# Kernel optimization log

Hardware: AMD Instinct MI355X
Metric: run time of the kernel (lower is better)

## Reference

```python
import jax, jax.numpy as jnp
import numpy as np

LTH_THOLD = 0.0

def _mlp(x, w1, b1, w2, b2, w3, b3):
    # x: [b,h,s,d]; w*: [h,in,out]; per-head 3-layer MLP with SiLU
    h1 = jax.nn.silu(jnp.einsum('bhsd,hde->bhse', x, w1) + b1[None, :, None, :])
    h2 = jax.nn.silu(jnp.einsum('bhsd,hde->bhse', h1, w2) + b2[None, :, None, :])
    return jnp.einsum('bhsd,hde->bhse', h2, w3) + b3[None, :, None, :]

def setup_inputs() -> dict:
    key = jax.random.key(0)
    ks = jax.random.split(key, 16)
    b, h, s, d, idim, fdim = 2, 32, 2048, 128, 128, 32
    sc1 = 1.0 / np.sqrt(d); sc2 = 1.0 / np.sqrt(idim)
    def lin(k, fan_in, shape, sc):
        return jax.random.uniform(k, shape, jnp.float32, -sc, sc)
    inp = {
        'K': jax.random.normal(ks[0], (b, h, s, d), jnp.float32),
        'Q': jax.random.normal(ks[1], (b, h, s, d), jnp.float32),
        'wk1': lin(ks[2], d, (h, d, idim), sc1), 'bk1': lin(ks[3], d, (h, idim), sc1),
        'wk2': lin(ks[4], idim, (h, idim, idim), sc2), 'bk2': lin(ks[5], idim, (h, idim), sc2),
        'wk3': lin(ks[6], idim, (h, idim, fdim), sc2), 'bk3': lin(ks[7], idim, (h, fdim), sc2),
        'wq1': lin(ks[8], d, (h, d, idim), sc1), 'bq1': lin(ks[9], d, (h, idim), sc1),
        'wq2': lin(ks[10], idim, (h, idim, idim), sc2), 'bq2': lin(ks[11], idim, (h, idim), sc2),
        'wq3': lin(ks[12], idim, (h, idim, fdim), sc2), 'bq3': lin(ks[13], idim, (h, fdim), sc2),
    }
    return inp

def reference(K, Q, wk1, bk1, wk2, bk2, wk3, bk3, wq1, bq1, wq2, bq2, wq3, bq3):
    Klift = jnp.tanh(_mlp(K, wk1, bk1, wk2, bk2, wk3, bk3))  # [b,h,sk,32]
    Qlift = jnp.tanh(_mlp(Q, wq1, bq1, wq2, bq2, wq3, bq3))  # [b,h,sq,32]
    scores = jnp.einsum('bhtd,bhsd->bhts', Qlift, Klift)      # [b,h,sq,sk]
    sq, sk = Qlift.shape[2], Klift.shape[2]
    causal = jnp.tril(jnp.ones((sq, sk), bool), k=sk - sq)
    mask_value = jnp.finfo(scores.dtype).min
    scores = jnp.where(causal[None, None], scores, mask_value)
    scores = jax.nn.sigmoid(scores - LTH_THOLD)
    return (scores, Klift)
```

## Files before the change

### kernel.cpp

```cpp
#include <hip/hip_runtime.h>

typedef __attribute__((ext_vector_type(8))) short bf16x8;
typedef __attribute__((ext_vector_type(4))) float f32x4;

#define MFMA(a,b,c) __builtin_amdgcn_mfma_f32_16x16x32_bf16(a,b,c,0,0,0)

static __device__ __forceinline__ unsigned short f2bf(float f){
  unsigned u = __float_as_uint(f);
  u += 0x7FFF + ((u>>16)&1);
  return (unsigned short)(u>>16);
}
static __device__ __forceinline__ float bf2f(unsigned short b){
  return __uint_as_float(((unsigned)b)<<16);
}

__global__ __launch_bounds__(256) void wswz(
    const float* __restrict__ wk1, const float* __restrict__ wk2, const float* __restrict__ wk3,
    const float* __restrict__ wq1, const float* __restrict__ wq2, const float* __restrict__ wq3,
    unsigned short* __restrict__ wb)
{
  int y = blockIdx.y;
  int net = y / 3, layer = y % 3;
  const float* src = net ? (layer==0?wq1: layer==1?wq2:wq3)
                         : (layer==0?wk1: layer==1?wk2:wk3);
  int N  = (layer==2) ? 32 : 128;
  int NT = N / 16;
  int total = 32 * NT * 4 * 64;
  int e = blockIdx.x * 256 + threadIdx.x;
  if (e >= total) return;
  int lane = e & 63;
  int ks   = (e >> 6) & 3;
  int nt   = (e >> 8) % NT;
  int h    = (e >> 8) / NT;
  int k0 = ks*32 + 8*(lane>>4);
  int n0 = nt*16 + (lane&15);
  const float* s = src + (size_t)h*128*N + (size_t)k0*N + n0;
  unsigned short hi[8], lo[8];
  #pragma unroll
  for (int j=0;j<8;++j){
    float v = s[(size_t)j*N];
    unsigned short hh = f2bf(v);
    hi[j] = hh;
    lo[j] = f2bf(v - bf2f(hh));
  }
  size_t nb   = (size_t)net * 2359296;
  size_t loff = (layer==0) ? 0 : (layer==1) ? 1048576 : 2097152;
  size_t losz = (layer==2) ? 131072 : 524288;
  size_t eidx = ((((size_t)h*NT + nt)*4 + ks)*64 + lane)*8;
  unsigned short* dH = wb + nb + loff + eidx;
  unsigned short* dL = dH + losz;
  *(bf16x8*)dH = *(const bf16x8*)hi;
  *(bf16x8*)dL = *(const bf16x8*)lo;
}

__global__ __launch_bounds__(256,3) void lift(
    const float* __restrict__ Kin, const float* __restrict__ Qin,
    const float* __restrict__ bk1, const float* __restrict__ bk2, const float* __restrict__ bk3,
    const float* __restrict__ bq1, const float* __restrict__ bq2, const float* __restrict__ bq3,
    const unsigned short* __restrict__ wb,
    unsigned short* __restrict__ qlift, unsigned short* __restrict__ klift,
    float* __restrict__ kout)
{
  __shared__ unsigned short XH[64][136];
  __shared__ unsigned short XL[64][136];
  int bid = blockIdx.x;
  int h   = (bid & 7)*4 + ((bid>>3)&3);
  int st  = (bid>>5) & 31;
  int bb  = (bid>>10) & 1;
  int net = bid>>11;
  size_t rowbase = (size_t)(bb*32 + h)*2048 + (size_t)st*64;
  const float* X = (net ? Qin : Kin) + rowbase*128;
  const unsigned short* wn = wb + (size_t)net*2359296;
  const float* b1 = (net ? bq1 : bk1) + h*128;
  const float* b2 = (net ? bq2 : bk2) + h*128;
  const float* b3 = (net ? bq3 : bk3) + h*32;
  unsigned short* lifto = net ? qlift : klift;

  int tid = threadIdx.x, w = tid >> 6, l = tid & 63;
  int lr = l & 15, lg = l >> 4;
  int acol0 = 8*lg;

  #pragma unroll
  for (int i=0;i<8;++i){
    int row = i*8 + (tid>>5);
    int col = (tid&31)*4;
    float4 v = *(const float4*)&X[(size_t)row*128 + col];
    unsigned u0=__float_as_uint(v.x), u1=__float_as_uint(v.y),
             u2=__float_as_uint(v.z), u3=__float_as_uint(v.w);
    float l0 = v.x - __uint_as_float(u0 & 0xFFFF0000u);
    float l1 = v.y - __uint_as_float(u1 & 0xFFFF0000u);
    float l2 = v.z - __uint_as_float(u2 & 0xFFFF0000u);
    float l3 = v.w - __uint_as_float(u3 & 0xFFFF0000u);
    *(uint2*)&XH[row][col] = make_uint2((u0>>16) | (u1 & 0xFFFF0000u),
                                        (u2>>16) | (u3 & 0xFFFF0000u));
    *(uint2*)&XL[row][col] = make_uint2((__float_as_uint(l0)>>16) | (__float_as_uint(l1) & 0xFFFF0000u),
                                        (__float_as_uint(l2)>>16) | (__float_as_uint(l3) & 0xFFFF0000u));
  }
  __syncthreads();

  for (int L=0; L<2; ++L){
    const unsigned short* wH = wn + (size_t)L*1048576;
    const unsigned short* wL = wH + 524288;
    const float* bias = L ? b2 : b1;
    f32x4 acc[2][4];
    #pragma unroll
    for (int ntl=0;ntl<2;++ntl)
      #pragma unroll
      for (int rt=0;rt<4;++rt)
        acc[ntl][rt] = (f32x4){0.f,0.f,0.f,0.f};

    #pragma unroll
    for (int ks=0;ks<4;++ks){
      bf16x8 bh[2], bl[2];
      #pragma unroll
      for (int ntl=0;ntl<2;++ntl){
        size_t eidx = ((((size_t)h*8 + (w*2+ntl))*4 + ks)*64 + l)*8;
        bh[ntl] = *(const bf16x8*)(wH + eidx);
        bl[ntl] = *(const bf16x8*)(wL + eidx);
      }
      #pragma unroll
      for (int rt=0;rt<4;++rt){
        bf16x8 ah = *(const bf16x8*)&XH[rt*16+lr][ks*32 + acol0];
        bf16x8 al = *(const bf16x8*)&XL[rt*16+lr][ks*32 + acol0];
        #pragma unroll
        for (int ntl=0;ntl<2;++ntl){
          f32x4 a = acc[ntl][rt];
          a = MFMA(bh[ntl], ah, a);
          a = MFMA(bh[ntl], al, a);
          a = MFMA(bl[ntl], ah, a);
          acc[ntl][rt] = a;
        }
      }
    }
    __syncthreads();
    #pragma unroll
    for (int ntl=0;ntl<2;++ntl){
      int n0 = (w*2+ntl)*16 + 4*lg;
      float4 bv = *(const float4*)&bias[n0];
      float bvv[4] = {bv.x, bv.y, bv.z, bv.w};
      #pragma unroll
      for (int rt=0;rt<4;++rt){
        int row = rt*16 + lr;
        unsigned hh[4], ll[4];
        #pragma unroll
        for (int i=0;i<4;++i){
          float v = acc[ntl][rt][i] + bvv[i];
          float sg = v * __builtin_amdgcn_rcpf(1.f + __expf(-v));
          unsigned u = __float_as_uint(sg);
          hh[i] = u >> 16;
          float lo = sg - __uint_as_float(u & 0xFFFF0000u);
          ll[i] = __float_as_uint(lo) >> 16;
        }
        *(uint2*)&XH[row][n0] = make_uint2(hh[0] | (hh[1]<<16), hh[2] | (hh[3]<<16));
        *(uint2*)&XL[row][n0] = make_uint2(ll[0] | (ll[1]<<16), ll[2] | (ll[3]<<16));
      }
    }
    __syncthreads();
  }

  {
    const unsigned short* wH = wn + 2097152;
    const unsigned short* wL = wH + 131072;
    int nt = w >> 1;
    int rb = (w & 1) * 2;
    f32x4 acc3[2];
    acc3[0] = (f32x4){0.f,0.f,0.f,0.f};
    acc3[1] = (f32x4){0.f,0.f,0.f,0.f};
    #pragma unroll
    for (int ks=0;ks<4;++ks){
      size_t eidx = ((((size_t)h*2 + nt)*4 + ks)*64 + l)*8;
      bf16x8 bh = *(const bf16x8*)(wH + eidx);
      bf16x8 bl = *(const bf16x8*)(wL + eidx);
      #pragma unroll
      for (int j=0;j<2;++j){
        bf16x8 ah = *(const bf16x8*)&XH[(rb+j)*16+lr][ks*32 + acol0];
        bf16x8 al = *(const bf16x8*)&XL[(rb+j)*16+lr][ks*32 + acol0];
        f32x4 a = acc3[j];
        a = MFMA(bh, ah, a);
        a = MFMA(bh, al, a);
        a = MFMA(bl, ah, a);
        acc3[j] = a;
      }
    }
    int n0 = nt*16 + 4*lg;
    float4 bv = *(const float4*)&b3[n0];
    float bvv[4] = {bv.x, bv.y, bv.z, bv.w};
    #pragma unroll
    for (int j=0;j<2;++j){
      int row = (rb+j)*16 + lr;
      float t4[4];
      unsigned short hb[4];
      #pragma unroll
      for (int i=0;i<4;++i){
        float v = acc3[j][i] + bvv[i];
        float e2 = __expf(2.f*v);
        float t  = 1.f - 2.f*__builtin_amdgcn_rcpf(e2 + 1.f);
        t4[i] = t;
        hb[i] = f2bf(t);
      }
      size_t gro = (rowbase + (size_t)row)*32 + n0;
      *(uint2*)&lifto[gro] = make_uint2((unsigned)hb[0] | ((unsigned)hb[1]<<16),
                                        (unsigned)hb[2] | ((unsigned)hb[3]<<16));
      if (net == 0)
        *(float4*)&kout[gro] = make_float4(t4[0], t4[1], t4[2], t4[3]);
    }
  }
}

__global__ __launch_bounds__(256) void scores_k(
    const unsigned short* __restrict__ qlift,
    const unsigned short* __restrict__ klift,
    float* __restrict__ out)
{
  int orig = blockIdx.x;
  int bid  = (orig & 7) * 2048 + (orig >> 3);
  int tc = bid & 15, tr = (bid >> 4) & 15, bh = bid >> 8;
  size_t sbase = (size_t)bh * 2048 * 2048;
  int r0 = tr * 128, c0 = tc * 128;
  int tid = threadIdx.x;

  if (tc > tr){
    float4 z = {0.f,0.f,0.f,0.f};
    #pragma unroll
    for (int it=0; it<16; ++it){
      int idx = it*256 + tid;
      int row = idx >> 5, c4 = idx & 31;
      *(float4*)&out[sbase + (size_t)(r0+row)*2048 + c0 + c4*4] = z;
    }
    return;
  }

  __shared__ float sbuf[4][16][128];
  int w = tid >> 6, l = tid & 63;
  int lr = l & 15, lg = l >> 4;
  int acol0 = 8*lg;
  float* sw = &sbuf[w][0][0];

  const unsigned short* qb = qlift + ((size_t)bh*2048 + r0 + w*32)*32;
  bf16x8 q0 = *(const bf16x8*)(qb + (size_t)lr*32 + acol0);
  bf16x8 q1 = *(const bf16x8*)(qb + (size_t)(16+lr)*32 + acol0);
  bool diag = (tc == tr);

  const unsigned short* kb = klift + ((size_t)bh*2048 + c0)*32;
  bf16x8 kf[8];
  #pragma unroll
  for (int st8=0; st8<8; ++st8)
    kf[st8] = *(const bf16x8*)(kb + (size_t)(st8*16+lr)*32 + acol0);

  #pragma unroll
  for (int pass=0; pass<2; ++pass){
    bf16x8 qf = pass ? q1 : q0;
    int tbase = r0 + w*32 + pass*16;
    int t = tbase + lr;

    #pragma unroll
    for (int st8=0; st8<8; ++st8){
      f32x4 z4 = {0.f,0.f,0.f,0.f};
      f32x4 d = MFMA(kf[st8], qf, z4);
      int scol = c0 + st8*16 + 4*lg;
      f32x4 p;
      #pragma unroll
      for (int i=0;i<4;++i){
        float pv = __builtin_amdgcn_rcpf(1.f + __expf(-d[i]));
        if (diag && (scol + i > t)) pv = 0.f;
        p[i] = pv;
      }
      int fi = (lr*128 + st8*16 + lg*4) ^ ((lr&7)<<2);
      *(f32x4*)&sw[fi] = p;
    }
    #pragma unroll
    for (int it=0; it<8; ++it){
      int r  = it*2 + (l>>5);
      int fi = (r*128 + (l&31)*4) ^ ((r&7)<<2);
      f32x4 v = *(const f32x4*)&sw[fi];
      *(f32x4*)&out[sbase + (size_t)(tbase + r)*2048 + c0 + (l&31)*4] = v;
    }
  }
}

extern "C" void kernel_launch(void* const* d_in, const int* in_sizes, int n_in,
                              void* d_out, int out_size, void* d_ws, size_t ws_size,
                              hipStream_t stream) {
  const float* K   = (const float*)d_in[0];
  const float* Q   = (const float*)d_in[1];
  const float* wk1 = (const float*)d_in[2];  const float* bk1 = (const float*)d_in[3];
  const float* wk2 = (const float*)d_in[4];  const float* bk2 = (const float*)d_in[5];
  const float* wk3 = (const float*)d_in[6];  const float* bk3 = (const float*)d_in[7];
  const float* wq1 = (const float*)d_in[8];  const float* bq1 = (const float*)d_in[9];
  const float* wq2 = (const float*)d_in[10]; const float* bq2 = (const float*)d_in[11];
  const float* wq3 = (const float*)d_in[12]; const float* bq3 = (const float*)d_in[13];
  float* out = (float*)d_out;

  unsigned short* ws    = (unsigned short*)d_ws;
  unsigned short* qlift = ws;
  unsigned short* klift = ws + 4194304;
  unsigned short* wbase = ws + 8388608;

  hipLaunchKernelGGL(wswz, dim3(256,6), dim3(256), 0, stream,
                     wk1, wk2, wk3, wq1, wq2, wq3, wbase);
  hipLaunchKernelGGL(lift, dim3(4096), dim3(256), 0, stream,
                     K, Q, bk1, bk2, bk3, bq1, bq2, bq3,
                     wbase, qlift, klift, out + 268435456ull);
  hipLaunchKernelGGL(scores_k, dim3(16384), dim3(256), 0, stream,
                     qlift, klift, out);
}
```

Baseline: 279.6 us.

## Remap scores kernel to row-strip blocks with waves striding column tiles

The scores kernel now gives each block a 16-row strip covering all 2048 columns. Each of the four waves walks every fourth 128-column tile, computing the causal tiles and writing zeros for the masked ones. Previously each block owned a 128x128 tile. The change balances causal versus zero-fill work within every block, so no blocks exist that only store zeros, and it halves the grid. The cost is that each wave reloads K fragments per tile from global memory, and Q reuse across the block drops.

```diff
diff --git a/kernel.cpp b/kernel.cpp
--- a/kernel.cpp
+++ b/kernel.cpp
@@ -213,67 +213,58 @@
     float* __restrict__ out)
 {
   int orig = blockIdx.x;
-  int bid  = (orig & 7) * 2048 + (orig >> 3);
-  int tc = bid & 15, tr = (bid >> 4) & 15, bh = bid >> 8;
-  size_t sbase = (size_t)bh * 2048 * 2048;
-  int r0 = tr * 128, c0 = tc * 128;
-  int tid = threadIdx.x;
-
-  if (tc > tr){
-    float4 z = {0.f,0.f,0.f,0.f};
-    #pragma unroll
-    for (int it=0; it<16; ++it){
-      int idx = it*256 + tid;
-      int row = idx >> 5, c4 = idx & 31;
-      *(float4*)&out[sbase + (size_t)(r0+row)*2048 + c0 + c4*4] = z;
-    }
-    return;
-  }
-
-  __shared__ float sbuf[4][16][128];
-  int w = tid >> 6, l = tid & 63;
+  int bid  = (orig & 7) * 1024 + (orig >> 3);
+  int sl = bid & 127;
+  int bh = bid >> 7;
+  int T0 = sl * 16;
+  int diagW = sl >> 3;
+  int tid = threadIdx.x, w = tid >> 6, l = tid & 63;
   int lr = l & 15, lg = l >> 4;
   int acol0 = 8*lg;
+
+  __shared__ float sbuf[4][16][128];
   float* sw = &sbuf[w][0][0];
 
-  const unsigned short* qb = qlift + ((size_t)bh*2048 + r0 + w*32)*32;
-  bf16x8 q0 = *(const bf16x8*)(qb + (size_t)lr*32 + acol0);
-  bf16x8 q1 = *(const bf16x8*)(qb + (size_t)(16+lr)*32 + acol0);
-  bool diag = (tc == tr);
-
-  const unsigned short* kb = klift + ((size_t)bh*2048 + c0)*32;
-  bf16x8 kf[8];
-  #pragma unroll
-  for (int st8=0; st8<8; ++st8)
-    kf[st8] = *(const bf16x8*)(kb + (size_t)(st8*16+lr)*32 + acol0);
-
-  #pragma unroll
-  for (int pass=0; pass<2; ++pass){
-    bf16x8 qf = pass ? q1 : q0;
-    int tbase = r0 + w*32 + pass*16;
-    int t = tbase + lr;
-
-    #pragma unroll
-    for (int st8=0; st8<8; ++st8){
-      f32x4 z4 = {0.f,0.f,0.f,0.f};
-      f32x4 d = MFMA(kf[st8], qf, z4);
-      int scol = c0 + st8*16 + 4*lg;
-      f32x4 p;
-      #pragma unroll
-      for (int i=0;i<4;++i){
-        float pv = __builtin_amdgcn_rcpf(1.f + __expf(-d[i]));
-        if (diag && (scol + i > t)) pv = 0.f;
-        p[i] = pv;
-      }
-      int fi = (lr*128 + st8*16 + lg*4) ^ ((lr&7)<<2);
-      *(f32x4*)&sw[fi] = p;
-    }
-    #pragma unroll
-    for (int it=0; it<8; ++it){
-      int r  = it*2 + (l>>5);
-      int fi = (r*128 + (l&31)*4) ^ ((r&7)<<2);
-      f32x4 v = *(const f32x4*)&sw[fi];
-      *(f32x4*)&out[sbase + (size_t)(tbase + r)*2048 + c0 + (l&31)*4] = v;
+  const unsigned short* qb = qlift + ((size_t)bh*2048 + T0)*32;
+  bf16x8 qf = *(const bf16x8*)(qb + (size_t)lr*32 + acol0);
+  const unsigned short* kbh = klift + (size_t)bh*2048*32;
+  size_t obase = (size_t)bh*4194304 + (size_t)T0*2048;
+  f32x4 z4 = {0.f,0.f,0.f,0.f};
+  int t = T0 + lr;
+
+  for (int W = w; W < 16; W += 4){
+    int c0 = W*128;
+    if (W <= diagW){
+      const unsigned short* kb = kbh + (size_t)c0*32;
+      bool dg = (W == diagW);
+      #pragma unroll
+      for (int st8=0; st8<8; ++st8){
+        bf16x8 kf = *(const bf16x8*)(kb + (size_t)(st8*16+lr)*32 + acol0);
+        f32x4 d = MFMA(kf, qf, z4);
+        int scol = c0 + st8*16 + 4*lg;
+        f32x4 p;
+        #pragma unroll
+        for (int i=0;i<4;++i){
+          float pv = __builtin_amdgcn_rcpf(1.f + __expf(-d[i]));
+          if (dg && (scol + i > t)) pv = 0.f;
+          p[i] = pv;
+        }
+        int fi = (lr*128 + st8*16 + lg*4) ^ ((lr&7)<<2);
+        *(f32x4*)&sw[fi] = p;
+      }
+      #pragma unroll
+      for (int it=0; it<8; ++it){
+        int r  = it*2 + (l>>5);
+        int fi = (r*128 + (l&31)*4) ^ ((r&7)<<2);
+        f32x4 v = *(const f32x4*)&sw[fi];
+        *(f32x4*)&out[obase + (size_t)r*2048 + c0 + (l&31)*4] = v;
+      }
+    } else {
+      #pragma unroll
+      for (int it=0; it<8; ++it){
+        int r = it*2 + (l>>5);
+        *(f32x4*)&out[obase + (size_t)r*2048 + c0 + (l&31)*4] = z4;
+      }
     }
   }
 }
@@ -301,6 +292,6 @@
   hipLaunchKernelGGL(lift, dim3(4096), dim3(256), 0, stream,
                      K, Q, bk1, bk2, bk3, bq1, bq2, bq3,
                      wbase, qlift, klift, out + 268435456ull);
-  hipLaunchKernelGGL(scores_k, dim3(16384), dim3(256), 0, stream,
+  hipLaunchKernelGGL(scores_k, dim3(8192), dim3(256), 0, stream,
                      qlift, klift, out);
 }
```

After: 286.7 us. +2.6%, slower.
